# Kernel tuning notes

Measured on AMD Instinct MI355X. Metric: run time of the kernel, lower is better.

## Reference

```python
import jax, jax.numpy as jnp
import numpy as np
from jax import lax

B, C_IN = 8192, 1

def _conv(x, w, b):
    # x: [N,C,H,W], w: [O,I,kh,kw] valid conv, stride 1
    y = lax.conv_general_dilated(x, w, window_strides=(1, 1), padding='VALID',
                                 dimension_numbers=('NCHW', 'OIHW', 'NCHW'))
    return y + b[None, :, None, None]

def _maxpool2(x):
    return lax.reduce_window(x, -jnp.inf, lax.max, (1, 1, 2, 2), (1, 1, 2, 2), 'VALID')

def setup_inputs() -> dict:
    key = jax.random.key(0)
    ks = jax.random.split(key, 9)
    def kaiming(k, shape, fan_in):
        return jax.random.normal(k, shape, jnp.float32) * np.float32(1.0 / np.sqrt(fan_in))
    x = jax.random.normal(ks[0], (B, C_IN, 28, 28), jnp.float32)
    w1 = kaiming(ks[1], (10, C_IN, 5, 5), C_IN * 25)
    b1 = kaiming(ks[2], (10,), C_IN * 25)
    w2 = kaiming(ks[3], (20, 10, 5, 5), 10 * 25)
    b2 = kaiming(ks[4], (20,), 10 * 25)
    wl1 = kaiming(ks[5], (50, 320), 320)
    bl1 = kaiming(ks[6], (50,), 320)
    wl2 = kaiming(ks[7], (10, 50), 50)
    bl2 = kaiming(ks[8], (10,), 50)
    return {"x": x, "w1": w1, "b1": b1, "w2": w2, "b2": b2,
            "wl1": wl1, "bl1": bl1, "wl2": wl2, "bl2": bl2}

def reference(x, w1, b1, w2, b2, wl1, bl1, wl2, bl2):
    h = jax.nn.relu(_conv(x, w1, b1))       # [B,10,24,24]
    h = _maxpool2(h)                         # [B,10,12,12]
    h = jax.nn.relu(_conv(h, w2, b2))        # [B,20,8,8]
    h = _maxpool2(h)                         # [B,20,4,4]
    h = h.reshape(h.shape[0], -1)            # [B,320]
    h = jax.nn.relu(h @ wl1.T + bl1)         # [B,50]
    return h @ wl2.T + bl2                   # [B,10]
```

## Files before the change

kernel.cpp:

```cpp
#include <hip/hip_runtime.h>

#define THREADS 256
#define IPB 4

typedef _Float16 f16;
typedef _Float16 f16x2 __attribute__((ext_vector_type(2)));
typedef _Float16 f16x4 __attribute__((ext_vector_type(4)));
typedef _Float16 f16x8 __attribute__((ext_vector_type(8)));
typedef float f32x2 __attribute__((ext_vector_type(2)));
typedef float f32x4 __attribute__((ext_vector_type(4)));
typedef float f32x16 __attribute__((ext_vector_type(16)));
typedef unsigned int uint;

__device__ __forceinline__ f16x2 pkrtz(float a, float b) {
    return __builtin_bit_cast(f16x2, __builtin_amdgcn_cvt_pkrtz(a, b));
}
template<int CTRL>
__device__ __forceinline__ float dppmax(float v) {
    const int i = __builtin_bit_cast(int, v);
    const int s = __builtin_amdgcn_update_dpp(i, i, CTRL, 0xF, 0xF, true);
    return fmaxf(v, __builtin_bit_cast(float, s));
}
__device__ __forceinline__ f16x8 ldpairs(const unsigned char* a) {
    const uint* p = (const uint*)a;
    uint4 u;
    u.x = p[0]; u.y = p[2]; u.z = p[4]; u.w = p[6];
    return __builtin_bit_cast(f16x8, u);
}

#define P1C 24
#define P1R 288
#define P1I 3456
#define XH  13824
#define XH_IMG 3136
#define SMEM_BYTES 20224

__global__ void pack_weights(const float* __restrict__ w1,
                             const float* __restrict__ w2,
                             const float* __restrict__ wl1,
                             unsigned char* __restrict__ ws) {
    f16x8* w2af = (f16x8*)(ws + 1024);
    f16x8* wl1pk = (f16x8*)(ws + 17408);
    const int gid = blockIdx.x * blockDim.x + threadIdx.x;
    const int gsz = gridDim.x * blockDim.x;
    for (int e = gid; e < 1000; e += gsz) {
        const int s = e / 40, r = e - s * 40;
        const int oc = r >> 1, h = r & 1;
        f16x8 a;
        #pragma unroll
        for (int j = 0; j < 8; ++j) {
            const int ic = h * 8 + j;
            a[j] = (f16)(ic < 10 ? w2[(oc * 10 + ic) * 25 + s] : 0.f);
        }
        w2af[e] = a;
    }
    for (int e = gid; e < 2560; e += gsz) {
        const int tile = e / 640, rem = e % 640;
        const int s = rem / 64, lane = rem % 64;
        const int m = lane & 15, quad = lane >> 4;
        const int hh = tile * 16 + m;
        f16x8 a;
        #pragma unroll
        for (int j = 0; j < 8; ++j)
            a[j] = (f16)(hh < 50 ? wl1[hh * 320 + s * 32 + quad * 8 + j] : 0.f);
        wl1pk[e] = a;
    }
}

__global__ __launch_bounds__(THREADS, 8)
void lenet_one(const float* __restrict__ x,
               const unsigned char* __restrict__ ws,
               const float* __restrict__ w1, const float* __restrict__ b1,
               const float* __restrict__ b2,
               const float* __restrict__ bl1,
               const float* __restrict__ wl2, const float* __restrict__ bl2,
               float* __restrict__ out, int batch)
{
    __shared__ __align__(16) unsigned char smem[SMEM_BYTES];
    f16*   p2h = (f16*)smem;
    float* h1  = (float*)(smem + 2624);

    const f16x8* w2af  = (const f16x8*)(ws + 1024);
    const f16x8* wl1pk = (const f16x8*)(ws + 17408);

    const int tid = threadIdx.x;
    const int lane = tid & 63;
    const int wv_ = tid >> 6;
    const int n15 = lane & 15;
    const int q4  = lane >> 4;
    const int cM = lane & 31, hK = lane >> 5;

    f16x8 A1 = {}, A2 = {};
    if (n15 < 10) {
        #pragma unroll
        for (int j = 0; j < 5; ++j) A1[j] = (f16)w1[n15 * 25 + q4 * 5 + j];
        if (q4 == 0) {
            #pragma unroll
            for (int j = 0; j < 5; ++j) A2[j] = (f16)w1[n15 * 25 + 20 + j];
        }
        if (q4 == 1) A2[0] = (f16)b1[n15];
    }

    #pragma unroll 1
    for (int sub = 0; sub < 2; ++sub) {
        if (tid < 112) {
            const int imL = tid / 56, rr = (tid % 56) >> 1, half = tid & 1;
            const int ig = min(blockIdx.x * IPB + sub * 2 + imL, batch - 1);
            const float* xp = x + (size_t)ig * 784 + rr * 28 + half * 14;
            float v[15];
            #pragma unroll
            for (int t = 0; t < 7; ++t) {
                const f32x2 a = *(const f32x2*)(xp + 2 * t);
                v[2 * t] = a[0]; v[2 * t + 1] = a[1];
            }
            v[14] = half ? 0.f : xp[14];
            uint* pw = (uint*)(smem + XH + imL * XH_IMG + rr * 112) + half * 14;
            #pragma unroll
            for (int t = 0; t < 7; ++t) {
                uint2 w;
                w.x = __builtin_bit_cast(uint, pkrtz(v[2 * t], v[2 * t + 1]));
                w.y = __builtin_bit_cast(uint, pkrtz(v[2 * t + 1], v[2 * t + 2]));
                *(uint2*)(pw + 2 * t) = w;
            }
        } else if (tid >= 224) {
            *(uint*)(smem + XH + 2 * XH_IMG + (tid - 224) * 4) = 0;
        }
        __syncthreads();

        #pragma unroll 1
        for (int i = 0; i < 12; ++i) {
            const int g = wv_ * 12 + i;
            const int imL = g / 24, rem = g % 24, u = rem >> 1, oxg = rem & 1;
            const int ox = oxg * 16 + n15;
            const unsigned char* pb = smem + XH + imL * XH_IMG + ox * 4;
            const int oy0 = 2 * u;
            const f16x8 B1a = ldpairs(pb + (oy0 + q4) * 112);
            const f16x8 B1b = ldpairs(pb + (oy0 + 1 + q4) * 112);
            f16x8 B2a = {}, B2b = {};
            if (q4 == 0) {
                B2a = ldpairs(pb + (oy0 + 4) * 112);
                B2b = ldpairs(pb + (oy0 + 5) * 112);
            } else if (q4 == 1) {
                B2a[0] = (f16)1.f; B2b[0] = (f16)1.f;
            }
            f32x4 aa = {0.f, 0.f, 0.f, 0.f}, ab = {0.f, 0.f, 0.f, 0.f};
            aa = __builtin_amdgcn_mfma_f32_16x16x32_f16(A1, B1a, aa, 0, 0, 0);
            ab = __builtin_amdgcn_mfma_f32_16x16x32_f16(A1, B1b, ab, 0, 0, 0);
            aa = __builtin_amdgcn_mfma_f32_16x16x32_f16(A2, B2a, aa, 0, 0, 0);
            ab = __builtin_amdgcn_mfma_f32_16x16x32_f16(A2, B2b, ab, 0, 0, 0);
            float vr[4];
            #pragma unroll
            for (int r = 0; r < 4; ++r) {
                float v = fmaxf(aa[r], ab[r]);
                v = dppmax<0xB1>(v);
                vr[r] = fmaxf(v, 0.f);
            }
            if (!(lane & 1) && q4 < 3 && (oxg == 0 || n15 < 8)) {
                const int im = sub * 2 + imL, px = oxg * 8 + (n15 >> 1);
                f16x2 o0, o1;
                o0[0] = (f16)vr[0]; o0[1] = (f16)vr[1];
                o1[0] = (f16)vr[2]; o1[1] = (f16)vr[3];
                uint2 w;
                w.x = __builtin_bit_cast(uint, o0);
                w.y = __builtin_bit_cast(uint, o1);
                *(uint2*)(smem + im * P1I + u * P1R + px * P1C + q4 * 8) = w;
            }
        }
        __syncthreads();
    }

    {
        const int cy = cM >> 3, cx = cM & 7;
        const int afoff = (cM < 20 ? cM : 19) * 2 + hK;
        int bb[2];
        #pragma unroll
        for (int q = 0; q < 2; ++q) {
            const int t = wv_ * 2 + q, im = t >> 1, h2 = t & 1;
            bb[q] = im * P1I + (4 * h2 + cy) * P1R + cx * P1C + hK * 16;
        }
        f32x16 acc[2];
        #pragma unroll
        for (int q = 0; q < 2; ++q)
            #pragma unroll
            for (int r = 0; r < 16; ++r) acc[q][r] = 0.f;
        #pragma unroll 1
        for (int ky = 0; ky < 5; ++ky) {
            #pragma unroll
            for (int kx = 0; kx < 5; ++kx) {
                const f16x8 a = w2af[(ky * 5 + kx) * 40 + afoff];
                #pragma unroll
                for (int q = 0; q < 2; ++q) {
                    const unsigned char* ad = smem + bb[q] + ky * P1R + kx * P1C;
                    const f16x4 lo = *(const f16x4*)(ad);
                    const f16x4 hi = *(const f16x4*)(ad + 8);
                    f16x8 b;
                    #pragma unroll
                    for (int j = 0; j < 4; ++j) { b[j] = lo[j]; b[4 + j] = hi[j]; }
                    acc[q] = __builtin_amdgcn_mfma_f32_32x32x16_f16(a, b, acc[q],
                                                                    0, 0, 0);
                }
            }
        }
        __syncthreads();
        #pragma unroll
        for (int q = 0; q < 2; ++q) {
            const int t = wv_ * 2 + q, im = t >> 1, h2 = t & 1;
            #pragma unroll
            for (int r = 0; r < 16; ++r) {
                const int m = (r & 3) + 8 * (r >> 2) + 4 * hK;
                float v = acc[q][r];
                v = dppmax<0xB1>(v);
                v = dppmax<0x128>(v);
                if (m < 20 && (lane & 9) == 0) {
                    const int py = 2 * h2 + (cM >> 4), px = cx >> 1;
                    p2h[im * 328 + m * 16 + py * 4 + px] =
                        (f16)fmaxf(v + b2[m], 0.f);
                }
            }
        }
    }
    __syncthreads();

    {
        f32x4 facc = {0.f, 0.f, 0.f, 0.f};
        #pragma unroll 1
        for (int s = 0; s < 10; ++s) {
            const f16x8 a = wl1pk[(wv_ * 10 + s) * 64 + lane];
            f16x8 b = {};
            if (n15 < IPB)
                b = *(const f16x8*)(p2h + n15 * 328 + s * 32 + q4 * 8);
            facc = __builtin_amdgcn_mfma_f32_16x16x32_f16(a, b, facc, 0, 0, 0);
        }
        if (n15 < IPB) {
            #pragma unroll
            for (int r = 0; r < 4; ++r) {
                const int h = wv_ * 16 + q4 * 4 + r;
                if (h < 50)
                    h1[n15 * 52 + h] = fmaxf(facc[r] + bl1[h], 0.f);
            }
        }
    }
    __syncthreads();

    if (tid < IPB * 10) {
        const int im = tid / 10, o = tid % 10;
        const int imgo = min(blockIdx.x * IPB + im, batch - 1);
        float a = bl2[o];
        #pragma unroll
        for (int h = 0; h < 50; ++h)
            a += h1[im * 52 + h] * wl2[o * 50 + h];
        out[(size_t)imgo * 10 + o] = a;
    }
}

extern "C" void kernel_launch(void* const* d_in, const int* in_sizes, int n_in,
                              void* d_out, int out_size, void* d_ws, size_t ws_size,
                              hipStream_t stream) {
    const float* x   = (const float*)d_in[0];
    const float* w1  = (const float*)d_in[1];
    const float* b1  = (const float*)d_in[2];
    const float* w2  = (const float*)d_in[3];
    const float* b2  = (const float*)d_in[4];
    const float* wl1 = (const float*)d_in[5];
    const float* bl1 = (const float*)d_in[6];
    const float* wl2 = (const float*)d_in[7];
    const float* bl2 = (const float*)d_in[8];
    float* out = (float*)d_out;
    unsigned char* ws = (unsigned char*)d_ws;

    const int batch = in_sizes[0] / 784;
    pack_weights<<<64, 256, 0, stream>>>(w1, w2, wl1, ws);
    const int grid = (batch + IPB - 1) / IPB;
    lenet_one<<<grid, THREADS, 0, stream>>>(x, ws, w1, b1, b2, bl1, wl2, bl2,
                                            out, batch);
}
```

Before: 124.4 us.

## Interleave conv1 input rows across images and reuse loaded B rows across iterations

The fp16 input staging layout now interleaves the two images per row (row stride 224 bytes) instead of storing them as separate image slabs. Each wave now owns a fixed image and column half and walks all 12 output row pairs in an unrolled descending loop. The B operands loaded for one row pair are kept in registers and reused as the second-MFMA operands four rows later, which roughly halves LDS reads for conv1. The cost is more live VGPRs and a fully unrolled loop, which may raise register pressure and reduce occupancy.

```diff
diff --git a/kernel.cpp b/kernel.cpp
--- a/kernel.cpp
+++ b/kernel.cpp
@@ -32,7 +32,6 @@
 #define P1R 288
 #define P1I 3456
 #define XH  13824
-#define XH_IMG 3136
 #define SMEM_BYTES 20224
 
 __global__ void pack_weights(const float* __restrict__ w1,
@@ -104,7 +103,7 @@
     #pragma unroll 1
     for (int sub = 0; sub < 2; ++sub) {
         if (tid < 112) {
-            const int imL = tid / 56, rr = (tid % 56) >> 1, half = tid & 1;
+            const int rr = tid >> 2, imL = (tid >> 1) & 1, half = tid & 1;
             const int ig = min(blockIdx.x * IPB + sub * 2 + imL, batch - 1);
             const float* xp = x + (size_t)ig * 784 + rr * 28 + half * 14;
             float v[15];
@@ -114,7 +113,7 @@
                 v[2 * t] = a[0]; v[2 * t + 1] = a[1];
             }
             v[14] = half ? 0.f : xp[14];
-            uint* pw = (uint*)(smem + XH + imL * XH_IMG + rr * 112) + half * 14;
+            uint* pw = (uint*)(smem + XH + rr * 224 + imL * 112) + half * 14;
             #pragma unroll
             for (int t = 0; t < 7; ++t) {
                 uint2 w;
@@ -123,47 +122,56 @@
                 *(uint2*)(pw + 2 * t) = w;
             }
         } else if (tid >= 224) {
-            *(uint*)(smem + XH + 2 * XH_IMG + (tid - 224) * 4) = 0;
+            *(uint*)(smem + XH + 28 * 224 + (tid - 224) * 4) = 0;
         }
         __syncthreads();
 
-        #pragma unroll 1
-        for (int i = 0; i < 12; ++i) {
-            const int g = wv_ * 12 + i;
-            const int imL = g / 24, rem = g % 24, u = rem >> 1, oxg = rem & 1;
+        {
+            const int imL = wv_ >> 1, oxg = wv_ & 1;
             const int ox = oxg * 16 + n15;
-            const unsigned char* pb = smem + XH + imL * XH_IMG + ox * 4;
-            const int oy0 = 2 * u;
-            const f16x8 B1a = ldpairs(pb + (oy0 + q4) * 112);
-            const f16x8 B1b = ldpairs(pb + (oy0 + 1 + q4) * 112);
-            f16x8 B2a = {}, B2b = {};
-            if (q4 == 0) {
-                B2a = ldpairs(pb + (oy0 + 4) * 112);
-                B2b = ldpairs(pb + (oy0 + 5) * 112);
-            } else if (q4 == 1) {
-                B2a[0] = (f16)1.f; B2b[0] = (f16)1.f;
-            }
-            f32x4 aa = {0.f, 0.f, 0.f, 0.f}, ab = {0.f, 0.f, 0.f, 0.f};
-            aa = __builtin_amdgcn_mfma_f32_16x16x32_f16(A1, B1a, aa, 0, 0, 0);
-            ab = __builtin_amdgcn_mfma_f32_16x16x32_f16(A1, B1b, ab, 0, 0, 0);
-            aa = __builtin_amdgcn_mfma_f32_16x16x32_f16(A2, B2a, aa, 0, 0, 0);
-            ab = __builtin_amdgcn_mfma_f32_16x16x32_f16(A2, B2b, ab, 0, 0, 0);
-            float vr[4];
-            #pragma unroll
-            for (int r = 0; r < 4; ++r) {
-                float v = fmaxf(aa[r], ab[r]);
-                v = dppmax<0xB1>(v);
-                vr[r] = fmaxf(v, 0.f);
-            }
-            if (!(lane & 1) && q4 < 3 && (oxg == 0 || n15 < 8)) {
-                const int im = sub * 2 + imL, px = oxg * 8 + (n15 >> 1);
-                f16x2 o0, o1;
-                o0[0] = (f16)vr[0]; o0[1] = (f16)vr[1];
-                o1[0] = (f16)vr[2]; o1[1] = (f16)vr[3];
-                uint2 w;
-                w.x = __builtin_bit_cast(uint, o0);
-                w.y = __builtin_bit_cast(uint, o1);
-                *(uint2*)(smem + im * P1I + u * P1R + px * P1C + q4 * 8) = w;
+            const int im = sub * 2 + imL;
+            const unsigned char* pb = smem + XH + imL * 112 + ox * 4
+                                    + q4 * 224;
+            unsigned char* wbase = smem + im * P1I;
+            f16x8 hA0 = {}, hB0 = {}, hA1 = {}, hB1 = {};
+            #pragma unroll
+            for (int uu = 0; uu < 12; ++uu) {
+                const int u = 11 - uu;
+                const f16x8 B1a = ldpairs(pb + (2 * u) * 224);
+                const f16x8 B1b = ldpairs(pb + (2 * u + 1) * 224);
+                f16x8 B2a, B2b;
+                if (u >= 10) {
+                    B2a = ldpairs(pb - q4 * 224 + (2 * u + 4) * 224);
+                    B2b = ldpairs(pb - q4 * 224 + (2 * u + 5) * 224);
+                } else {
+                    B2a = (u & 1) ? hA1 : hA0;
+                    B2b = (u & 1) ? hB1 : hB0;
+                }
+                if (u & 1) { hA1 = B1a; hB1 = B1b; }
+                else       { hA0 = B1a; hB0 = B1b; }
+                if (q4 == 1) { B2a[0] = (f16)1.f; B2b[0] = (f16)1.f; }
+                f32x4 aa = {0.f, 0.f, 0.f, 0.f}, ab = {0.f, 0.f, 0.f, 0.f};
+                aa = __builtin_amdgcn_mfma_f32_16x16x32_f16(A1, B1a, aa, 0, 0, 0);
+                ab = __builtin_amdgcn_mfma_f32_16x16x32_f16(A1, B1b, ab, 0, 0, 0);
+                aa = __builtin_amdgcn_mfma_f32_16x16x32_f16(A2, B2a, aa, 0, 0, 0);
+                ab = __builtin_amdgcn_mfma_f32_16x16x32_f16(A2, B2b, ab, 0, 0, 0);
+                float vr[4];
+                #pragma unroll
+                for (int r = 0; r < 4; ++r) {
+                    float v = fmaxf(aa[r], ab[r]);
+                    v = dppmax<0xB1>(v);
+                    vr[r] = fmaxf(v, 0.f);
+                }
+                if (!(lane & 1) && q4 < 3 && (oxg == 0 || n15 < 8)) {
+                    const int px = oxg * 8 + (n15 >> 1);
+                    f16x2 o0, o1;
+                    o0[0] = (f16)vr[0]; o0[1] = (f16)vr[1];
+                    o1[0] = (f16)vr[2]; o1[1] = (f16)vr[3];
+                    uint2 w;
+                    w.x = __builtin_bit_cast(uint, o0);
+                    w.y = __builtin_bit_cast(uint, o1);
+                    *(uint2*)(wbase + u * P1R + px * P1C + q4 * 8) = w;
+                }
             }
         }
         __syncthreads();
```

New measurement: 119.6 us. -3.9%, faster.
